# Optimization experiments

Hardware: AMD Instinct MI355X
Metric: run time of the kernel (lower is better)

Reference implementation:

```python
import jax, jax.numpy as jnp
import numpy as np

FILTER_SIZE = 8
INPUT_DIM = 128
KERNEL_SIZE = 256


def setup_inputs() -> dict:
    key = jax.random.key(0)
    k1, k2, k3, k4 = jax.random.split(key, 4)
    user_batch = jax.random.normal(k1, (32, 2048, INPUT_DIM), dtype=jnp.float32)
    # Params initialized like torch.rand (uniform [0,1))
    filt = jax.random.uniform(k2, (FILTER_SIZE, INPUT_DIM), dtype=jnp.float32)
    W_k = jax.random.uniform(k3, (FILTER_SIZE * INPUT_DIM, KERNEL_SIZE), dtype=jnp.float32)
    b_k = jax.random.uniform(k4, (KERNEL_SIZE,), dtype=jnp.float32)
    return {"user_batch": user_batch, "filt": filt, "W_k": W_k, "b_k": b_k}


def reference(user_batch, filt, W_k, b_k):
    B, L, D = user_batch.shape
    F = filt.shape[0]
    n_win = L - F  # NOTE: original loop is range(0, L - F): exactly L - F windows
    # Gather sliding windows: [B, n_win, F, D]
    idx = jnp.arange(n_win)[:, None] + jnp.arange(F)[None, :]
    windows = user_batch[:, idx, :]
    # Elementwise mul with filter then contract flattened (F*D) against W_k
    W = W_k.reshape(F, D, -1)  # [F, D, K]
    out = jnp.einsum('blfd,fd,fdk->blk', windows, filt, W)
    return jax.nn.relu(out + b_k)
```

## Files before the change

### kernel.cpp

```cpp
#include <hip/hip_runtime.h>


#define L_SZ   2048
#define NWIN   2040
#define BM     128
#define MT     16

typedef __attribute__((ext_vector_type(8))) short bf16x8;
typedef __attribute__((ext_vector_type(4))) short bf16x4;
typedef __attribute__((ext_vector_type(4))) float f32x4;

static __device__ __forceinline__ short f2bf(float f) {
    union { float f; unsigned u; } v; v.f = f;
    unsigned r = v.u + 0x7FFFu + ((v.u >> 16) & 1u);
    return (short)(r >> 16);
}

static __device__ __forceinline__ void gload_lds16(const short* g, short* l) {
    __builtin_amdgcn_global_load_lds(
        (const __attribute__((address_space(1))) unsigned int*)g,
        (__attribute__((address_space(3))) unsigned int*)l, 16, 0, 0);
}

__global__ __launch_bounds__(256) void prep_w_kernel(
    const float* __restrict__ Wk, const float* __restrict__ filt,
    short* __restrict__ wp2)
{
    int g   = blockIdx.x * 256 + threadIdx.x;
    int R   = g >> 11;
    int w   = g & 2047;
    int np  = w >> 3;
    int pos = w & 7;
    int cs  = pos ^ (np & 7);
    int kb  = R * 64 + cs * 8;
    bf16x8 o;
    #pragma unroll
    for (int jj = 0; jj < 8; ++jj)
        o[jj] = f2bf(Wk[(size_t)(kb + jj) * 256 + np] * filt[kb + jj]);
    *reinterpret_cast<bf16x8*>(&wp2[(size_t)g * 8]) = o;
}

__global__ __launch_bounds__(512, 4) void cnn_enc_kernel(
    const float* __restrict__ ub, const short* __restrict__ wp2,
    const float* __restrict__ bk, float* __restrict__ out)
{
    __shared__ short sA[135 * 136];
    __shared__ short sB[16384];

    const int tid   = threadIdx.x;
    const int bid   = blockIdx.x;
    const int mt    = bid & 15;
    const int batch = bid >> 4;
    const int l0    = mt * BM;

    for (int idx = tid; idx < 135 * 32; idx += 512) {
        int r  = idx >> 5;
        int dc = idx & 31;
        int rg = l0 + r; if (rg > L_SZ - 1) rg = L_SZ - 1;
        const float4 v = *reinterpret_cast<const float4*>(
            ub + (((size_t)batch * L_SZ + rg) << 7) + (dc << 2));
        bf16x4 o;
        o.x = f2bf(v.x); o.y = f2bf(v.y); o.z = f2bf(v.z); o.w = f2bf(v.w);
        *reinterpret_cast<bf16x4*>(&sA[r * 136 + (dc << 2)]) = o;
    }

    const int lane = tid & 63;
    const int wave = tid >> 6;
    const int wm   = wave >> 2;
    const int wn   = wave & 3;
    const int t16  = lane & 15;
    const int quad = lane >> 4;

    f32x4 acc[4][4];
    #pragma unroll
    for (int i = 0; i < 4; ++i)
        #pragma unroll
        for (int j = 0; j < 4; ++j)
            acc[i][j] = (f32x4){0.f, 0.f, 0.f, 0.f};

    int aoff[4];
    #pragma unroll
    for (int i = 0; i < 4; ++i)
        aoff[i] = (wm * 64 + i * 16 + t16) * 136 + quad * 8;
    int bnp[4];
    #pragma unroll
    for (int j = 0; j < 4; ++j)
        bnp[j] = wn * 64 + j * 16 + t16;

    __syncthreads();

    #pragma unroll 1
    for (int chunk = 0; chunk < 16; ++chunk) {
        const short* wpbase = wp2 + (size_t)chunk * 16384;
        #pragma unroll
        for (int r = 0; r < 4; ++r) {
            int ubase = r * 512 + wave * 64;
            gload_lds16(wpbase + (ubase + lane) * 8, &sB[ubase * 8]);
        }
        __syncthreads();

        #pragma unroll
        for (int s = 0; s < 2; ++s) {
            const int step = (chunk << 1) | s;
            const int f = step >> 2, sd = step & 3;
            bf16x8 a[4], b[4];
            #pragma unroll
            for (int i = 0; i < 4; ++i)
                a[i] = *reinterpret_cast<const bf16x8*>(
                    &sA[aoff[i] + f * 136 + sd * 32]);
            #pragma unroll
            for (int j = 0; j < 4; ++j) {
                int np = bnp[j];
                int cs = s * 4 + quad;
                b[j] = *reinterpret_cast<const bf16x8*>(
                    &sB[(np * 8 + (cs ^ (np & 7))) * 8]);
            }
            #pragma unroll
            for (int i = 0; i < 4; ++i)
                #pragma unroll
                for (int j = 0; j < 4; ++j)
                    acc[i][j] = __builtin_amdgcn_mfma_f32_16x16x32_bf16(
                        a[i], b[j], acc[i][j], 0, 0, 0);
        }
        __syncthreads();
    }

    #pragma unroll
    for (int j = 0; j < 4; ++j) {
        int n_glob = wn * 64 + j * 16 + t16;
        float bias = bk[n_glob];
        #pragma unroll
        for (int i = 0; i < 4; ++i) {
            #pragma unroll
            for (int r = 0; r < 4; ++r) {
                int l = l0 + wm * 64 + i * 16 + quad * 4 + r;
                if (l < NWIN) {
                    float v = acc[i][j][r] + bias;
                    out[((size_t)batch * NWIN + l) * 256 + n_glob] =
                        v > 0.f ? v : 0.f;
                }
            }
        }
    }
}

extern "C" void kernel_launch(void* const* d_in, const int* in_sizes, int n_in,
                              void* d_out, int out_size, void* d_ws, size_t ws_size,
                              hipStream_t stream) {
    const float* ub   = (const float*)d_in[0];
    const float* filt = (const float*)d_in[1];
    const float* Wk   = (const float*)d_in[2];
    const float* bk   = (const float*)d_in[3];
    float* out = (float*)d_out;
    short* wp2 = (short*)d_ws;

    hipLaunchKernelGGL(prep_w_kernel, dim3(128), dim3(256), 0, stream,
                       Wk, filt, wp2);
    hipLaunchKernelGGL(cnn_enc_kernel, dim3(32 * MT), dim3(512), 0, stream,
                       ub, wp2, bk, out);
}
```

Before: 127.4 us.

## Double-buffer weight chunks, stage input in slices, and widen per-wave N tile

```diff
diff --git a/kernel.cpp b/kernel.cpp
--- a/kernel.cpp
+++ b/kernel.cpp
@@ -27,12 +27,12 @@
     short* __restrict__ wp2)
 {
     int g   = blockIdx.x * 256 + threadIdx.x;
-    int R   = g >> 11;
-    int w   = g & 2047;
-    int np  = w >> 3;
-    int pos = w & 7;
-    int cs  = pos ^ (np & 7);
-    int kb  = R * 64 + cs * 8;
+    int R   = g >> 10;
+    int w   = g & 1023;
+    int np  = w >> 2;
+    int pos = w & 3;
+    int cs  = pos ^ ((np >> 1) & 3);
+    int kb  = R * 32 + cs * 8;
     bf16x8 o;
     #pragma unroll
     for (int jj = 0; jj < 8; ++jj)
@@ -40,94 +40,97 @@
     *reinterpret_cast<bf16x8*>(&wp2[(size_t)g * 8]) = o;
 }
 
-__global__ __launch_bounds__(512, 4) void cnn_enc_kernel(
+__global__ __launch_bounds__(256, 2) void cnn_enc_kernel(
     const float* __restrict__ ub, const short* __restrict__ wp2,
     const float* __restrict__ bk, float* __restrict__ out)
 {
     __shared__ short sA[135 * 136];
-    __shared__ short sB[16384];
+    __shared__ short sB[2 * 8192];
 
     const int tid   = threadIdx.x;
     const int bid   = blockIdx.x;
     const int mt    = bid & 15;
     const int batch = bid >> 4;
+    const int rot   = (bid >> 8) << 4;
     const int l0    = mt * BM;
-
-    for (int idx = tid; idx < 135 * 32; idx += 512) {
-        int r  = idx >> 5;
-        int dc = idx & 31;
-        int rg = l0 + r; if (rg > L_SZ - 1) rg = L_SZ - 1;
-        const float4 v = *reinterpret_cast<const float4*>(
-            ub + (((size_t)batch * L_SZ + rg) << 7) + (dc << 2));
-        bf16x4 o;
-        o.x = f2bf(v.x); o.y = f2bf(v.y); o.z = f2bf(v.z); o.w = f2bf(v.w);
-        *reinterpret_cast<bf16x4*>(&sA[r * 136 + (dc << 2)]) = o;
-    }
 
     const int lane = tid & 63;
     const int wave = tid >> 6;
-    const int wm   = wave >> 2;
-    const int wn   = wave & 3;
+    const int wm   = wave >> 1;
+    const int wn   = wave & 1;
     const int t16  = lane & 15;
     const int quad = lane >> 4;
 
-    f32x4 acc[4][4];
+    auto stageA = [&](int s) {
+        for (int idx = tid; idx < 135 * 8; idx += 256) {
+            int r  = idx >> 3;
+            int c4 = idx & 7;
+            int rg = l0 + r; if (rg > L_SZ - 1) rg = L_SZ - 1;
+            const float4 v = *reinterpret_cast<const float4*>(
+                ub + (((size_t)batch * L_SZ + rg) << 7) + s * 32 + c4 * 4);
+            bf16x4 o;
+            o.x = f2bf(v.x); o.y = f2bf(v.y); o.z = f2bf(v.z); o.w = f2bf(v.w);
+            *reinterpret_cast<bf16x4*>(&sA[r * 136 + s * 32 + c4 * 4]) = o;
+        }
+    };
+    auto stageB = [&](int c, int buf) {
+        const short* wpb = wp2 + (size_t)c * 8192;
+        #pragma unroll
+        for (int r = 0; r < 4; ++r) {
+            int ubase = r * 256 + wave * 64;
+            gload_lds16(wpb + (ubase + lane) * 8, &sB[buf * 8192 + ubase * 8]);
+        }
+    };
+
+    f32x4 acc[4][8];
     #pragma unroll
     for (int i = 0; i < 4; ++i)
         #pragma unroll
-        for (int j = 0; j < 4; ++j)
+        for (int j = 0; j < 8; ++j)
             acc[i][j] = (f32x4){0.f, 0.f, 0.f, 0.f};
 
     int aoff[4];
     #pragma unroll
     for (int i = 0; i < 4; ++i)
         aoff[i] = (wm * 64 + i * 16 + t16) * 136 + quad * 8;
-    int bnp[4];
+    int bpos[8];
     #pragma unroll
-    for (int j = 0; j < 4; ++j)
-        bnp[j] = wn * 64 + j * 16 + t16;
+    for (int j = 0; j < 8; ++j) {
+        int np = wn * 128 + j * 16 + t16;
+        bpos[j] = np * 32 + (quad ^ ((np >> 1) & 3)) * 8;
+    }
 
+    stageA(0);
+    stageB(rot, 0);
     __syncthreads();
 
     #pragma unroll 1
-    for (int chunk = 0; chunk < 16; ++chunk) {
-        const short* wpbase = wp2 + (size_t)chunk * 16384;
+    for (int c = 0; c < 32; ++c) {
+        if (c < 3)  stageA(c + 1);
+        if (c < 31) stageB((c + 1 + rot) & 31, (c + 1) & 1);
+        const int ce = (c + rot) & 31;
+        const int f  = ce >> 2, ds = ce & 3;
+        const int bb = (c & 1) * 8192;
+        bf16x8 a[4], b[8];
         #pragma unroll
-        for (int r = 0; r < 4; ++r) {
-            int ubase = r * 512 + wave * 64;
-            gload_lds16(wpbase + (ubase + lane) * 8, &sB[ubase * 8]);
-        }
-        __syncthreads();
-
+        for (int i = 0; i < 4; ++i)
+            a[i] = *reinterpret_cast<const bf16x8*>(
+                &sA[aoff[i] + f * 136 + ds * 32]);
         #pragma unroll
-        for (int s = 0; s < 2; ++s) {
-            const int step = (chunk << 1) | s;
-            const int f = step >> 2, sd = step & 3;
-            bf16x8 a[4], b[4];
+        for (int j = 0; j < 8; ++j)
+            b[j] = *reinterpret_cast<const bf16x8*>(&sB[bb + bpos[j]]);
+        #pragma unroll
+        for (int i = 0; i < 4; ++i)
             #pragma unroll
-            for (int i = 0; i < 4; ++i)
-                a[i] = *reinterpret_cast<const bf16x8*>(
-                    &sA[aoff[i] + f * 136 + sd * 32]);
-            #pragma unroll
-            for (int j = 0; j < 4; ++j) {
-                int np = bnp[j];
-                int cs = s * 4 + quad;
-                b[j] = *reinterpret_cast<const bf16x8*>(
-                    &sB[(np * 8 + (cs ^ (np & 7))) * 8]);
-            }
-            #pragma unroll
-            for (int i = 0; i < 4; ++i)
-                #pragma unroll
-                for (int j = 0; j < 4; ++j)
-                    acc[i][j] = __builtin_amdgcn_mfma_f32_16x16x32_bf16(
-                        a[i], b[j], acc[i][j], 0, 0, 0);
-        }
+            for (int j = 0; j < 8; ++j)
+                acc[i][j] = __builtin_amdgcn_mfma_f32_16x16x32_bf16(
+                    a[i], b[j], acc[i][j], 0, 0, 0);
         __syncthreads();
     }
 
     #pragma unroll
-    for (int j = 0; j < 4; ++j) {
-        int n_glob = wn * 64 + j * 16 + t16;
+    for (int j = 0; j < 8; ++j) {
+        int n_glob = wn * 128 + j * 16 + t16;
         float bias = bk[n_glob];
         #pragma unroll
         for (int i = 0; i < 4; ++i) {
@@ -156,6 +159,6 @@
 
     hipLaunchKernelGGL(prep_w_kernel, dim3(128), dim3(256), 0, stream,
                        Wk, filt, wp2);
-    hipLaunchKernelGGL(cnn_enc_kernel, dim3(32 * MT), dim3(512), 0, stream,
+    hipLaunchKernelGGL(cnn_enc_kernel, dim3(32 * MT), dim3(256), 0, stream,
                        ub, wp2, bk, out);
 }
```

New measurement: 134.6 us. 5.6% more time.
